# Performance work log

Measured on AMD Instinct MI355X. Metric: run time of the kernel, lower is better.

The kernel has to match this reference:

```python
import jax, jax.numpy as jnp
import numpy as np

B, M, T, N = 128, 256, 512, 512

def setup_inputs() -> dict:
    key = jax.random.key(0)
    ks = jax.random.split(key, 6)
    return {
        "hidden_state": jax.random.normal(ks[0], (B, M), jnp.float32),
        "cell_state": jax.random.normal(ks[1], (B, M), jnp.float32),
        "X": jax.random.normal(ks[2], (B, T, N), jnp.float32),
        "We1": jax.random.normal(ks[3], (2 * M, T), jnp.float32) * 0.05,
        "be1": jnp.zeros((T,), jnp.float32),
        "We2": jax.random.normal(ks[4], (T, T), jnp.float32) * 0.05,
        "be2": jnp.zeros((T,), jnp.float32),
        "v": jax.random.normal(ks[5], (T, 1), jnp.float32) * 0.05,
        "bv": jnp.zeros((1,), jnp.float32),
    }

def reference(hidden_state, cell_state, X, We1, be1, We2, be2, v, bv):
    # concat hidden + cell: [B, 2m]; Dense(T) then broadcast over n (K.repeat)
    hc = jnp.concatenate([hidden_state, cell_state], axis=-1)
    hs = (hc @ We1 + be1)[:, None, :]                 # [B, 1, T] (broadcast over n)
    # Permute X -> [B, n, T], Dense(T): contract over T
    ux = jnp.einsum('btn,tk->bnk', X, We2) + be2      # [B, n, T]
    # add + tanh + Dense(1) fused chain
    e = jnp.tanh(hs + ux) @ v + bv                    # [B, n, 1]
    # Permute -> [B, 1, n], softmax over last axis (n)
    attn = jax.nn.softmax(jnp.swapaxes(e, 1, 2), axis=-1)  # [B, 1, n]
    return attn
```

## Files before the change

kernel.cpp:

```cpp
#include <hip/hip_runtime.h>
#include <hip/hip_bf16.h>


typedef _Float16 half8 __attribute__((ext_vector_type(8)));
typedef float floatx4 __attribute__((ext_vector_type(4)));

__device__ __forceinline__ float fast_tanh(float x) {
    float cx = fminf(15.0f, fmaxf(-15.0f, x));
    float e = __expf(2.0f * cx);
    return (e - 1.0f) * __fdividef(1.0f, e + 1.0f);
}

__global__ __launch_bounds__(256) void k_prep_a(const float* __restrict__ We2,
                                                _Float16* __restrict__ Af) {
    __shared__ float w2[32][512];
    const int ts = blockIdx.x;
    for (int idx = threadIdx.x; idx < 32 * 512; idx += 256) {
        int tl = idx >> 9, k = idx & 511;
        w2[tl][k] = We2[(ts * 32 + tl) * 512 + k];
    }
    __syncthreads();
    for (int item = threadIdx.x; item < 32 * 64; item += 256) {
        int c = item >> 6, l = item & 63;
        int k  = c * 16 + (l & 15);
        int tl = (l >> 4) * 8;
        half8 h;
#pragma unroll
        for (int j = 0; j < 8; ++j) h[j] = (_Float16)w2[tl + j][k];
        *(half8*)&Af[(((size_t)ts * 32 + c) * 64 + l) * 8] = h;
    }
}

__global__ __launch_bounds__(256) void k_hs(const float* __restrict__ hidden,
                                            const float* __restrict__ cell,
                                            const float* __restrict__ We1,
                                            const float* __restrict__ be1,
                                            const float* __restrict__ be2,
                                            float* __restrict__ g) {
    __shared__ __align__(16) float hcl[8][512];
    __shared__ float red[4][8][64];
    const int b0 = (blockIdx.x >> 3) << 3;
    const int k0 = (blockIdx.x & 7) << 6;
    for (int idx = threadIdx.x; idx < 8 * 512; idx += 256) {
        int bi = idx >> 9, j = idx & 511;
        hcl[bi][j] = (j < 256) ? hidden[(b0 + bi) * 256 + j]
                               : cell[(b0 + bi) * 256 + j - 256];
    }
    __syncthreads();
    const int kl = threadIdx.x & 63;
    const int jc = threadIdx.x >> 6;
    const int k  = k0 + kl;
    float acc[8] = {};
    for (int j = jc * 128; j < jc * 128 + 128; j += 4) {
        float w0 = We1[(j + 0) * 512 + k];
        float w1 = We1[(j + 1) * 512 + k];
        float w2 = We1[(j + 2) * 512 + k];
        float w3 = We1[(j + 3) * 512 + k];
#pragma unroll
        for (int bi = 0; bi < 8; ++bi) {
            float4 h = *(const float4*)&hcl[bi][j];
            acc[bi] += h.x * w0 + h.y * w1 + h.z * w2 + h.w * w3;
        }
    }
#pragma unroll
    for (int bi = 0; bi < 8; ++bi) red[jc][bi][kl] = acc[bi];
    __syncthreads();
    for (int idx = threadIdx.x; idx < 512; idx += 256) {
        int bi = idx >> 6, kk = idx & 63;
        float s = red[0][bi][kk] + red[1][bi][kk] + red[2][bi][kk] + red[3][bi][kk];
        int kg = k0 + kk;
        g[(b0 + bi) * 512 + kg] = s + be1[kg] + be2[kg];
    }
}

__global__ __launch_bounds__(256, 3) void k_main(const float* __restrict__ X,
                                                 const _Float16* __restrict__ Af,
                                                 const float* __restrict__ g,
                                                 const float* __restrict__ vvec,
                                                 float* __restrict__ Ep) {
    __shared__ __align__(16) _Float16 Xb[2][2048];
    const int tid  = threadIdx.x;
    const int lane = tid & 63;
    const int wv   = tid >> 6;
    const int l16  = lane & 15;
    const int lhi  = lane >> 4;
    const int logical = (blockIdx.x & 7) * 256 + (blockIdx.x >> 3);
    const int kblk = logical & 1;
    const int nt   = (logical >> 1) & 7;
    const int b    = logical >> 4;
    const int n0   = nt << 6;

    const float* Xg = X + (size_t)b * 262144 + n0;
    const _Float16* Ag = Af + (size_t)(kblk * 16 + wv * 4) * 512 + (size_t)lane * 8;

    const int xn = tid & 63;
    const int xo = tid >> 6;
    const float* Xt = Xg + (size_t)(xo * 8) * 512 + xn;
    const int wslot = xn * 32 + ((xo ^ (xn & 3) ^ ((xn >> 2) & 3)) << 3);
    int roff[4];
#pragma unroll
    for (int nf = 0; nf < 4; ++nf) {
        int n = nf * 16 + l16;
        roff[nf] = n * 32 + ((lhi ^ (n & 3) ^ ((n >> 2) & 3)) << 3);
    }

    float xs0[8], xs1[8], xs2[8];
#define XLOAD(s_, arr_)                                                        \
    do { _Pragma("unroll")                                                     \
         for (int j = 0; j < 8; ++j)                                           \
             arr_[j] = Xt[(size_t)(s_) * 16384 + (size_t)j * 512];             \
    } while (0)
#define XSTORE(s_, arr_)                                                       \
    do { half8 h;                                                              \
         _Pragma("unroll")                                                     \
         for (int j = 0; j < 8; ++j) h[j] = (_Float16)arr_[j];                 \
         *(half8*)&Xb[(s_) & 1][wslot] = h;                                    \
    } while (0)
#define ALOAD(s_, arr_)                                                        \
    do { _Pragma("unroll")                                                     \
         for (int kf = 0; kf < 4; ++kf)                                        \
             arr_[kf] = *(const half8*)(Ag + (size_t)(s_) * 16384 +            \
                                        (size_t)kf * 512);                     \
    } while (0)

    half8 afA[4], afB[4];

    XLOAD(0, xs0);
    XLOAD(1, xs1);
    XLOAD(2, xs2);
    ALOAD(0, afA);
    XSTORE(0, xs0);
    asm volatile("s_waitcnt lgkmcnt(0)" ::: "memory");
    __builtin_amdgcn_sched_barrier(0);
    __builtin_amdgcn_s_barrier();
    __builtin_amdgcn_sched_barrier(0);

    floatx4 acc[4][4];
#pragma unroll
    for (int a = 0; a < 4; ++a)
#pragma unroll
        for (int c = 0; c < 4; ++c) acc[a][c] = (floatx4){0.f, 0.f, 0.f, 0.f};

#pragma unroll
    for (int s = 0; s < 16; ++s) {
        const int cur = s & 1;
        if (s + 1 < 16) {
            if ((s & 1) == 0) ALOAD(s + 1, afB);
            else              ALOAD(s + 1, afA);
        }
        if (s + 3 < 16) {
            if ((s % 3) == 0)      XLOAD(s + 3, xs0);
            else if ((s % 3) == 1) XLOAD(s + 3, xs1);
            else                   XLOAD(s + 3, xs2);
        }
        __builtin_amdgcn_sched_barrier(0);
        half8 bf[4];
#pragma unroll
        for (int nf = 0; nf < 4; ++nf)
            bf[nf] = *(const half8*)&Xb[cur][roff[nf]];
        if (s + 1 < 16) {
            if (((s + 1) % 3) == 0)      XSTORE(s + 1, xs0);
            else if (((s + 1) % 3) == 1) XSTORE(s + 1, xs1);
            else                         XSTORE(s + 1, xs2);
        }
        __builtin_amdgcn_s_setprio(1);
        if ((s & 1) == 0) {
#pragma unroll
            for (int kf = 0; kf < 4; ++kf)
#pragma unroll
                for (int nf = 0; nf < 4; ++nf)
                    acc[kf][nf] = __builtin_amdgcn_mfma_f32_16x16x32_f16(
                        afA[kf], bf[nf], acc[kf][nf], 0, 0, 0);
        } else {
#pragma unroll
            for (int kf = 0; kf < 4; ++kf)
#pragma unroll
                for (int nf = 0; nf < 4; ++nf)
                    acc[kf][nf] = __builtin_amdgcn_mfma_f32_16x16x32_f16(
                        afB[kf], bf[nf], acc[kf][nf], 0, 0, 0);
        }
        __builtin_amdgcn_s_setprio(0);
        asm volatile("s_waitcnt lgkmcnt(0)" ::: "memory");
        __builtin_amdgcn_sched_barrier(0);
        __builtin_amdgcn_s_barrier();
        __builtin_amdgcn_sched_barrier(0);
    }
#undef XLOAD
#undef XSTORE
#undef ALOAD

    const float* gb = g + b * 512;
    float sacc[4] = {0.f, 0.f, 0.f, 0.f};
#pragma unroll
    for (int kf = 0; kf < 4; ++kf) {
        const int kb = kblk * 256 + wv * 64 + kf * 16 + lhi * 4;
        float g0 = gb[kb + 0], g1 = gb[kb + 1], g2 = gb[kb + 2], g3 = gb[kb + 3];
        float v0 = vvec[kb + 0], v1 = vvec[kb + 1], v2 = vvec[kb + 2], v3 = vvec[kb + 3];
#pragma unroll
        for (int nf = 0; nf < 4; ++nf) {
            sacc[nf] += fast_tanh(acc[kf][nf][0] + g0) * v0;
            sacc[nf] += fast_tanh(acc[kf][nf][1] + g1) * v1;
            sacc[nf] += fast_tanh(acc[kf][nf][2] + g2) * v2;
            sacc[nf] += fast_tanh(acc[kf][nf][3] + g3) * v3;
        }
    }
#pragma unroll
    for (int nf = 0; nf < 4; ++nf) {
        sacc[nf] += __shfl_xor(sacc[nf], 16);
        sacc[nf] += __shfl_xor(sacc[nf], 32);
    }
    __syncthreads();
    float* ered = (float*)&Xb[0][0];
    if (lane < 16) {
#pragma unroll
        for (int nf = 0; nf < 4; ++nf) ered[wv * 64 + nf * 16 + l16] = sacc[nf];
    }
    __syncthreads();
    if (tid < 64) {
        float e = ered[tid] + ered[64 + tid] + ered[128 + tid] + ered[192 + tid];
        Ep[(size_t)kblk * 65536 + b * 512 + n0 + tid] = e;
    }
}

__global__ __launch_bounds__(256) void k_softmax(const float* __restrict__ Ep,
                                                 float* __restrict__ out) {
    __shared__ float rmax[4], rsum[4];
    const int b = blockIdx.x;
    const int tid = threadIdx.x;
    const float* E0 = Ep;
    const float* E1 = Ep + 65536;
    float e0 = E0[b * 512 + tid] + E1[b * 512 + tid];
    float e1 = E0[b * 512 + 256 + tid] + E1[b * 512 + 256 + tid];
    float m = fmaxf(e0, e1);
    for (int o = 32; o > 0; o >>= 1) m = fmaxf(m, __shfl_xor(m, o));
    if ((tid & 63) == 0) rmax[tid >> 6] = m;
    __syncthreads();
    m = fmaxf(fmaxf(rmax[0], rmax[1]), fmaxf(rmax[2], rmax[3]));
    float p0 = __expf(e0 - m), p1 = __expf(e1 - m);
    float ss = p0 + p1;
    for (int o = 32; o > 0; o >>= 1) ss += __shfl_xor(ss, o);
    if ((tid & 63) == 0) rsum[tid >> 6] = ss;
    __syncthreads();
    ss = rsum[0] + rsum[1] + rsum[2] + rsum[3];
    float inv = __fdividef(1.0f, ss);
    out[b * 512 + tid] = p0 * inv;
    out[b * 512 + 256 + tid] = p1 * inv;
}

extern "C" void kernel_launch(void* const* d_in, const int* in_sizes, int n_in,
                              void* d_out, int out_size, void* d_ws, size_t ws_size,
                              hipStream_t stream) {
    const float* hidden = (const float*)d_in[0];
    const float* cell   = (const float*)d_in[1];
    const float* X      = (const float*)d_in[2];
    const float* We1    = (const float*)d_in[3];
    const float* be1    = (const float*)d_in[4];
    const float* We2    = (const float*)d_in[5];
    const float* be2    = (const float*)d_in[6];
    const float* v      = (const float*)d_in[7];
    float* out = (float*)d_out;

    char* ws = (char*)d_ws;
    _Float16* Af = (_Float16*)ws;
    float* g     = (float*)(ws + 524288);
    float* Ep    = (float*)(ws + 786432);

    k_prep_a<<<16, 256, 0, stream>>>(We2, Af);
    k_hs<<<128, 256, 0, stream>>>(hidden, cell, We1, be1, be2, g);
    k_main<<<2048, 256, 0, stream>>>(X, Af, g, v, Ep);
    k_softmax<<<128, 256, 0, stream>>>(Ep, out);
}
```

Baseline: 76.83 us.

## Stage whole X tile in LDS with larger 512-thread blocks covering all T

Each block now covers 128 n-columns across the full 512-wide T contraction and both k halves, using eight waves split 2x4 over n and k. The entire 512x128 X slab is converted to fp16 and stored in a 128 KB LDS buffer up front, which removes the per-step double-buffer barriers. The kblk split and its partial-sum buffer disappear, so X is read once per (b,n) instead of twice. The cost is one block per CU, heavy LDS use, and a serial load phase before any MFMA work, so memory and compute no longer overlap within a block.

```diff
diff --git a/kernel.cpp b/kernel.cpp
--- a/kernel.cpp
+++ b/kernel.cpp
@@ -73,127 +73,112 @@
     }
 }
 
-__global__ __launch_bounds__(256, 3) void k_main(const float* __restrict__ X,
+__global__ __launch_bounds__(512, 1) void k_main(const float* __restrict__ X,
                                                  const _Float16* __restrict__ Af,
                                                  const float* __restrict__ g,
                                                  const float* __restrict__ vvec,
-                                                 float* __restrict__ Ep) {
-    __shared__ __align__(16) _Float16 Xb[2][2048];
+                                                 float* __restrict__ E) {
+    __shared__ __align__(16) _Float16 Xb[65536];
     const int tid  = threadIdx.x;
     const int lane = tid & 63;
     const int wv   = tid >> 6;
     const int l16  = lane & 15;
     const int lhi  = lane >> 4;
-    const int logical = (blockIdx.x & 7) * 256 + (blockIdx.x >> 3);
-    const int kblk = logical & 1;
-    const int nt   = (logical >> 1) & 7;
-    const int b    = logical >> 4;
-    const int n0   = nt << 6;
+    const int wn   = wv >> 2;
+    const int wk   = wv & 3;
+    const int logical = (blockIdx.x & 7) * 64 + (blockIdx.x >> 3);
+    const int nt   = logical & 3;
+    const int b    = logical >> 2;
+    const int n0   = nt << 7;
 
     const float* Xg = X + (size_t)b * 262144 + n0;
-    const _Float16* Ag = Af + (size_t)(kblk * 16 + wv * 4) * 512 + (size_t)lane * 8;
-
-    const int xn = tid & 63;
-    const int xo = tid >> 6;
-    const float* Xt = Xg + (size_t)(xo * 8) * 512 + xn;
-    const int wslot = xn * 32 + ((xo ^ (xn & 3) ^ ((xn >> 2) & 3)) << 3);
-    int roff[4];
-#pragma unroll
-    for (int nf = 0; nf < 4; ++nf) {
-        int n = nf * 16 + l16;
-        roff[nf] = n * 32 + ((lhi ^ (n & 3) ^ ((n >> 2) & 3)) << 3);
-    }
-
-    float xs0[8], xs1[8], xs2[8];
-#define XLOAD(s_, arr_)                                                        \
-    do { _Pragma("unroll")                                                     \
-         for (int j = 0; j < 8; ++j)                                           \
-             arr_[j] = Xt[(size_t)(s_) * 16384 + (size_t)j * 512];             \
-    } while (0)
-#define XSTORE(s_, arr_)                                                       \
-    do { half8 h;                                                              \
-         _Pragma("unroll")                                                     \
-         for (int j = 0; j < 8; ++j) h[j] = (_Float16)arr_[j];                 \
-         *(half8*)&Xb[(s_) & 1][wslot] = h;                                    \
-    } while (0)
+    const _Float16* Ag = Af + (size_t)(wk * 8) * 512 + (size_t)lane * 8;
+
+    {
+        const int xn = tid & 127;
+        const int xq = tid >> 7;
+        const float* Xt = Xg + (size_t)(xq * 8) * 512 + xn;
+        const int slotb = ((xn >> 4) * 64 + (xq << 4) + (xn & 15)) * 8;
+        float xsA[8], xsB[8];
+#define XSLOAD(s_, arr_)                                                       \
+        do { _Pragma("unroll")                                                 \
+             for (int j = 0; j < 8; ++j)                                       \
+                 arr_[j] = Xt[(size_t)((s_) * 32 + j) * 512];                  \
+        } while (0)
+#define XSSTORE(s_, arr_)                                                      \
+        do { half8 h;                                                          \
+             _Pragma("unroll")                                                 \
+             for (int j = 0; j < 8; ++j) h[j] = (_Float16)arr_[j];             \
+             *(half8*)&Xb[(s_) * 4096 + slotb] = h;                            \
+        } while (0)
+        XSLOAD(0, xsA);
+#pragma unroll
+        for (int ts = 0; ts < 16; ++ts) {
+            if (ts + 1 < 16) {
+                if (((ts + 1) & 1) == 0) XSLOAD(ts + 1, xsA);
+                else                     XSLOAD(ts + 1, xsB);
+            }
+            if ((ts & 1) == 0) XSSTORE(ts, xsA);
+            else               XSSTORE(ts, xsB);
+        }
+#undef XSLOAD
+#undef XSSTORE
+    }
+    __syncthreads();
+
+    floatx4 acc[8][4];
+#pragma unroll
+    for (int a = 0; a < 8; ++a)
+#pragma unroll
+        for (int c = 0; c < 4; ++c) acc[a][c] = (floatx4){0.f, 0.f, 0.f, 0.f};
+
+    half8 afA[8], afB[8];
 #define ALOAD(s_, arr_)                                                        \
     do { _Pragma("unroll")                                                     \
-         for (int kf = 0; kf < 4; ++kf)                                        \
+         for (int kf = 0; kf < 8; ++kf)                                        \
              arr_[kf] = *(const half8*)(Ag + (size_t)(s_) * 16384 +            \
                                         (size_t)kf * 512);                     \
     } while (0)
-
-    half8 afA[4], afB[4];
-
-    XLOAD(0, xs0);
-    XLOAD(1, xs1);
-    XLOAD(2, xs2);
     ALOAD(0, afA);
-    XSTORE(0, xs0);
-    asm volatile("s_waitcnt lgkmcnt(0)" ::: "memory");
-    __builtin_amdgcn_sched_barrier(0);
-    __builtin_amdgcn_s_barrier();
-    __builtin_amdgcn_sched_barrier(0);
-
-    floatx4 acc[4][4];
-#pragma unroll
-    for (int a = 0; a < 4; ++a)
-#pragma unroll
-        for (int c = 0; c < 4; ++c) acc[a][c] = (floatx4){0.f, 0.f, 0.f, 0.f};
 
 #pragma unroll
     for (int s = 0; s < 16; ++s) {
-        const int cur = s & 1;
         if (s + 1 < 16) {
             if ((s & 1) == 0) ALOAD(s + 1, afB);
             else              ALOAD(s + 1, afA);
         }
-        if (s + 3 < 16) {
-            if ((s % 3) == 0)      XLOAD(s + 3, xs0);
-            else if ((s % 3) == 1) XLOAD(s + 3, xs1);
-            else                   XLOAD(s + 3, xs2);
-        }
         __builtin_amdgcn_sched_barrier(0);
-        half8 bf[4];
+        half8 xf[4];
 #pragma unroll
         for (int nf = 0; nf < 4; ++nf)
-            bf[nf] = *(const half8*)&Xb[cur][roff[nf]];
-        if (s + 1 < 16) {
-            if (((s + 1) % 3) == 0)      XSTORE(s + 1, xs0);
-            else if (((s + 1) % 3) == 1) XSTORE(s + 1, xs1);
-            else                         XSTORE(s + 1, xs2);
-        }
+            xf[nf] = *(const half8*)
+                &Xb[((s * 8 + wn * 4 + nf) * 64 + lane) * 8];
         __builtin_amdgcn_s_setprio(1);
         if ((s & 1) == 0) {
 #pragma unroll
-            for (int kf = 0; kf < 4; ++kf)
+            for (int kf = 0; kf < 8; ++kf)
 #pragma unroll
                 for (int nf = 0; nf < 4; ++nf)
                     acc[kf][nf] = __builtin_amdgcn_mfma_f32_16x16x32_f16(
-                        afA[kf], bf[nf], acc[kf][nf], 0, 0, 0);
+                        afA[kf], xf[nf], acc[kf][nf], 0, 0, 0);
         } else {
 #pragma unroll
-            for (int kf = 0; kf < 4; ++kf)
+            for (int kf = 0; kf < 8; ++kf)
 #pragma unroll
                 for (int nf = 0; nf < 4; ++nf)
                     acc[kf][nf] = __builtin_amdgcn_mfma_f32_16x16x32_f16(
-                        afB[kf], bf[nf], acc[kf][nf], 0, 0, 0);
+                        afB[kf], xf[nf], acc[kf][nf], 0, 0, 0);
         }
         __builtin_amdgcn_s_setprio(0);
-        asm volatile("s_waitcnt lgkmcnt(0)" ::: "memory");
         __builtin_amdgcn_sched_barrier(0);
-        __builtin_amdgcn_s_barrier();
-        __builtin_amdgcn_sched_barrier(0);
-    }
-#undef XLOAD
-#undef XSTORE
+    }
 #undef ALOAD
 
     const float* gb = g + b * 512;
     float sacc[4] = {0.f, 0.f, 0.f, 0.f};
 #pragma unroll
-    for (int kf = 0; kf < 4; ++kf) {
-        const int kb = kblk * 256 + wv * 64 + kf * 16 + lhi * 4;
+    for (int kf = 0; kf < 8; ++kf) {
+        const int kb = wk * 128 + kf * 16 + lhi * 4;
         float g0 = gb[kb + 0], g1 = gb[kb + 1], g2 = gb[kb + 2], g3 = gb[kb + 3];
         float v0 = vvec[kb + 0], v1 = vvec[kb + 1], v2 = vvec[kb + 2], v3 = vvec[kb + 3];
 #pragma unroll
@@ -210,27 +195,26 @@
         sacc[nf] += __shfl_xor(sacc[nf], 32);
     }
     __syncthreads();
-    float* ered = (float*)&Xb[0][0];
+    float* ered = (float*)&Xb[0];
     if (lane < 16) {
 #pragma unroll
-        for (int nf = 0; nf < 4; ++nf) ered[wv * 64 + nf * 16 + l16] = sacc[nf];
-    }
-    __syncthreads();
-    if (tid < 64) {
-        float e = ered[tid] + ered[64 + tid] + ered[128 + tid] + ered[192 + tid];
-        Ep[(size_t)kblk * 65536 + b * 512 + n0 + tid] = e;
-    }
-}
-
-__global__ __launch_bounds__(256) void k_softmax(const float* __restrict__ Ep,
+        for (int nf = 0; nf < 4; ++nf)
+            ered[wk * 128 + wn * 64 + nf * 16 + l16] = sacc[nf];
+    }
+    __syncthreads();
+    if (tid < 128) {
+        float e = ered[tid] + ered[128 + tid] + ered[256 + tid] + ered[384 + tid];
+        E[b * 512 + n0 + tid] = e;
+    }
+}
+
+__global__ __launch_bounds__(256) void k_softmax(const float* __restrict__ E,
                                                  float* __restrict__ out) {
     __shared__ float rmax[4], rsum[4];
     const int b = blockIdx.x;
     const int tid = threadIdx.x;
-    const float* E0 = Ep;
-    const float* E1 = Ep + 65536;
-    float e0 = E0[b * 512 + tid] + E1[b * 512 + tid];
-    float e1 = E0[b * 512 + 256 + tid] + E1[b * 512 + 256 + tid];
+    float e0 = E[b * 512 + tid];
+    float e1 = E[b * 512 + 256 + tid];
     float m = fmaxf(e0, e1);
     for (int o = 32; o > 0; o >>= 1) m = fmaxf(m, __shfl_xor(m, o));
     if ((tid & 63) == 0) rmax[tid >> 6] = m;
@@ -263,10 +247,10 @@
     char* ws = (char*)d_ws;
     _Float16* Af = (_Float16*)ws;
     float* g     = (float*)(ws + 524288);
-    float* Ep    = (float*)(ws + 786432);
+    float* E     = (float*)(ws + 786432);
 
     k_prep_a<<<16, 256, 0, stream>>>(We2, Af);
     k_hs<<<128, 256, 0, stream>>>(hidden, cell, We1, be1, be2, g);
-    k_main<<<2048, 256, 0, stream>>>(X, Af, g, v, Ep);
-    k_softmax<<<128, 256, 0, stream>>>(Ep, out);
-}
+    k_main<<<512, 512, 0, stream>>>(X, Af, g, v, E);
+    k_softmax<<<128, 256, 0, stream>>>(E, out);
+}
```

Result: slower. 85.51 us (+11.3%).
